# Kernel tuning notes

Hardware: AMD Instinct MI355X
Metric: run time of the kernel (lower is better)

The kernel has to match this reference:

```python
import jax, jax.numpy as jnp
import numpy as np

B, T, C = 64, 256, 64
E, H, HB, OUT = 32, 64, 128, 2


def setup_inputs() -> dict:
    key = jax.random.key(0)
    ks = iter(jax.random.split(key, 32))
    s = 0.02
    p = {}
    p["x"] = jax.random.normal(next(ks), (B, T, C), jnp.float32)
    # embedding Linear(1, E)
    p["embed_w"] = jax.random.normal(next(ks), (E, 1), jnp.float32) * s
    p["embed_b"] = jnp.zeros((E,), jnp.float32)
    # GRU (input E, hidden H); gate order r,z,n
    p["w_ih"] = jax.random.normal(next(ks), (3 * H, E), jnp.float32) * s
    p["w_hh"] = jax.random.normal(next(ks), (3 * H, H), jnp.float32) * s
    p["b_ih"] = jnp.zeros((3 * H,), jnp.float32)
    p["b_hh"] = jnp.zeros((3 * H,), jnp.float32)
    # BTP query / key MLPs: H->HB->HB->HB
    for nm in ("q", "k"):
        p[f"{nm}1_w"] = jax.random.normal(next(ks), (HB, H), jnp.float32) * s
        p[f"{nm}1_b"] = jnp.zeros((HB,), jnp.float32)
        p[f"{nm}2_w"] = jax.random.normal(next(ks), (HB, HB), jnp.float32) * s
        p[f"{nm}2_b"] = jnp.zeros((HB,), jnp.float32)
        p[f"{nm}3_w"] = jax.random.normal(next(ks), (HB, HB), jnp.float32) * s
        p[f"{nm}3_b"] = jnp.zeros((HB,), jnp.float32)
    # Gate bias (n_components x n_components), torch.randn init
    p["gate_bias"] = jax.random.normal(next(ks), (C, C), jnp.float32)
    # classifier: C^2 -> C^2/2 -> C^2/4 -> OUT
    d0, d1, d2 = C * C, C * C // 2, C * C // 4
    p["clf1_w"] = jax.random.normal(next(ks), (d1, d0), jnp.float32) * s
    p["clf1_b"] = jnp.zeros((d1,), jnp.float32)
    p["clf2_w"] = jax.random.normal(next(ks), (d2, d1), jnp.float32) * s
    p["clf2_b"] = jnp.zeros((d2,), jnp.float32)
    p["clf3_w"] = jax.random.normal(next(ks), (OUT, d2), jnp.float32) * s
    p["clf3_b"] = jnp.zeros((OUT,), jnp.float32)
    # predictor Linear(H, 1)
    p["pred_w"] = jax.random.normal(next(ks), (1, H), jnp.float32) * s
    p["pred_b"] = jnp.zeros((1,), jnp.float32)
    return p


def _mlp3(h, w1, b1, w2, b2, w3, b3):
    h = jax.nn.relu(h @ w1.T + b1)
    h = jax.nn.relu(h @ w2.T + b2)
    return h @ w3.T + b3


def reference(x, embed_w, embed_b, w_ih, w_hh, b_ih, b_hh,
              q1_w, q1_b, q2_w, q2_b, q3_w, q3_b,
              k1_w, k1_b, k2_w, k2_b, k3_w, k3_b,
              gate_bias, clf1_w, clf1_b, clf2_w, clf2_b, clf3_w, clf3_b,
              pred_w, pred_b):
    Bb, Tt, Cc = x.shape
    Hh = w_hh.shape[1]
    # embeddings: Linear(1,E) applied to each scalar -> [B,C,T,E]
    embedded = x.transpose(0, 2, 1)[..., None] * embed_w[:, 0] + embed_b
    xs = jnp.moveaxis(embedded, 2, 0)  # [T,B,C,E]

    def gru_cell(h, xt):
        gi = xt @ w_ih.T + b_ih           # [B,C,3H]
        gh = h @ w_hh.T + b_hh
        gi_r, gi_z, gi_n = jnp.split(gi, 3, axis=-1)
        gh_r, gh_z, gh_n = jnp.split(gh, 3, axis=-1)
        r = jax.nn.sigmoid(gi_r + gh_r)
        z = jax.nn.sigmoid(gi_z + gh_z)
        n = jnp.tanh(gi_n + r * gh_n)
        return (1.0 - z) * n + z * h

    def btp(h):
        q = _mlp3(h, q1_w, q1_b, q2_w, q2_b, q3_w, q3_b)   # [B,C,HB]
        k = _mlp3(h, k1_w, k1_b, k2_w, k2_b, k3_w, k3_b)
        transfer = jnp.einsum('bqd,bkd->bqk', q, k)        # [B,C,C]
        norms = jnp.sqrt(jnp.sum(transfer * transfer, axis=(1, 2), keepdims=True))
        transfer = transfer / norms
        gate = jax.nn.sigmoid(jnp.abs(transfer) + gate_bias)
        transfer = transfer * gate
        next_states = jnp.einsum('bij,bjd->bid', transfer, h)
        return next_states, transfer

    def step(h, xt):
        h = gru_cell(h, xt)
        h, transfer = btp(h)
        return h, (h, transfer)

    h0 = jnp.zeros((Bb, Cc, Hh), x.dtype)
    _, (hs, mats) = jax.lax.scan(step, h0, xs)
    hidden_states = jnp.moveaxis(hs, 0, 1)    # [B,T,C,H]
    matrices = jnp.moveaxis(mats, 0, 1)       # [B,T,C,C]

    # predictor on hidden states at t=0..T-2 -> predicts x[:,1:,:]
    predicted = (hidden_states[:, :-1] @ pred_w.T + pred_b)[..., 0]  # [B,T-1,C]

    clf_in = matrices.reshape(Bb, Tt, Cc * Cc)
    h1 = jax.nn.relu(clf_in @ clf1_w.T + clf1_b)   # dropout is identity in eval
    h2 = jax.nn.relu(h1 @ clf2_w.T + clf2_b)
    time_logits = h2 @ clf3_w.T + clf3_b            # [B,T,OUT]
    logits = jnp.mean(time_logits, axis=1)          # [B,OUT]
    return logits, matrices, time_logits, predicted, x[:, 1:, :]
```

## Files before the change

kernel.cpp:

```cpp
#include <hip/hip_runtime.h>
#include <hip/hip_bf16.h>
#include <math.h>

#define B_BATCH 64
#define T_STEPS 256
#define C_COMP  64

#define WSW_BYTE_OFF 2048
#define WHH_OFF 0
#define Q1_OFF 12288
#define K1_OFF 20480
#define Q2_OFF 28672
#define K2_OFF 45056
#define Q3_OFF 61440
#define K3_OFF 77824
#define C1WB_BYTE 262144
#define C2WB_BYTE 17039360
#define H1B_BYTE  21233664
#define H2B_BYTE  88342528
#define MB16_BYTE 121896960ULL

#define MAT_OFF  128
#define TL_OFF   67108992
#define PRED_OFF 67141760
#define XC_OFF   68186240

#define GST 196
#define HS  68
#define TS  68
#define GBS 68

typedef __attribute__((ext_vector_type(8))) short short8;
typedef __attribute__((ext_vector_type(4))) float f32x4;
#define MFMA16(a,b,c) __builtin_amdgcn_mfma_f32_16x16x32_bf16(a,b,c,0,0,0)

__device__ __forceinline__ float fsigm(float v) {
    return __builtin_amdgcn_rcpf(1.0f + __expf(-v));
}
__device__ __forceinline__ float ftanh(float v) {
    return 1.0f - 2.0f * __builtin_amdgcn_rcpf(__expf(2.0f * v) + 1.0f);
}
__device__ __forceinline__ short f2bs(float f) {
    unsigned u = __float_as_uint(f);
    u += 0x7fffu + ((u >> 16) & 1u);
    return (short)(u >> 16);
}
__device__ __forceinline__ float bf2f(short s) {
    return __uint_as_float(((unsigned)(unsigned short)s) << 16);
}
__device__ __forceinline__ unsigned pk2(float a, float b) {
    return (unsigned)(unsigned short)f2bs(a) | ((unsigned)(unsigned short)f2bs(b) << 16);
}
__device__ __forceinline__ void bar_lds() {
    asm volatile("s_waitcnt lgkmcnt(0)" ::: "memory");
    __builtin_amdgcn_s_barrier();
}
__device__ __forceinline__ int xorr(int row) { return ((row >> 1) & 7) << 3; }

__device__ __forceinline__ void async16(void* lds, const void* g) {
    __builtin_amdgcn_global_load_lds((const __attribute__((address_space(1))) void*)g,
                                     (__attribute__((address_space(3))) void*)lds, 16, 0, 0);
}

__global__ void precompute_kernel(const float* __restrict__ w_ih,
                                  const float* __restrict__ embed_w,
                                  const float* __restrict__ embed_b,
                                  const float* __restrict__ b_ih,
                                  float* __restrict__ avec, float* __restrict__ cvec)
{
    int g = threadIdx.x;
    if (g < 192) {
        float a = 0.f, c = 0.f;
        for (int e = 0; e < 32; ++e) {
            float w = w_ih[g * 32 + e];
            a += w * embed_w[e];
            c += w * embed_b[e];
        }
        avec[g] = a;
        cvec[g] = c + b_ih[g];
    }
}

__global__ void tobf16_kernel(const float* __restrict__ src, short* __restrict__ dst, int n)
{
    int i = blockIdx.x * 256 + threadIdx.x;
    if (i < n) dst[i] = f2bs(src[i]);
}

__global__ void expand_kernel(const short* __restrict__ mb, float* __restrict__ mat)
{
    const size_t i = ((size_t)blockIdx.x * 256 + threadIdx.x) * 8;
    short8 v = *(const short8*)&mb[i];
    float4 lo, hi;
    lo.x = bf2f(v[0]); lo.y = bf2f(v[1]); lo.z = bf2f(v[2]); lo.w = bf2f(v[3]);
    hi.x = bf2f(v[4]); hi.y = bf2f(v[5]); hi.z = bf2f(v[6]); hi.w = bf2f(v[7]);
    *reinterpret_cast<float4*>(&mat[i])     = lo;
    *reinterpret_cast<float4*>(&mat[i + 4]) = hi;
}

template<int KST, int AST, bool RELU>
__device__ __forceinline__ void two_strip_sw(
    const short* __restrict__ A,
    const short8* __restrict__ B0, const short8* __restrict__ B1,
    const f32x4 bias0, const f32x4 bias1,
    short* __restrict__ outb, const int s0, const int s1, const int ln, const int lh)
{
    f32x4 acc0[4], acc1[4];
#pragma unroll
    for (int g = 0; g < 4; ++g) { acc0[g] = bias0; acc1[g] = bias1; }
#pragma unroll
    for (int kk = 0; kk < KST; ++kk)
#pragma unroll
        for (int g = 0; g < 4; ++g) {
            const int row = g * 16 + ln;
            short8 a = *(const short8*)&A[row * AST + ((kk * 32 + lh * 8) ^ xorr(row))];
            acc0[g] = MFMA16(B0[kk], a, acc0[g]);
            acc1[g] = MFMA16(B1[kk], a, acc1[g]);
        }
#pragma unroll
    for (int g = 0; g < 4; ++g) {
        const int row = g * 16 + ln;
        f32x4 v0 = acc0[g], v1 = acc1[g];
        if (RELU) {
#pragma unroll
            for (int q = 0; q < 4; ++q) { v0[q] = fmaxf(v0[q], 0.f); v1[q] = fmaxf(v1[q], 0.f); }
        }
        uint2 p0, p1;
        p0.x = pk2(v0[0], v0[1]); p0.y = pk2(v0[2], v0[3]);
        p1.x = pk2(v1[0], v1[1]); p1.y = pk2(v1[2], v1[3]);
        *(uint2*)&outb[row * 128 + ((s0 * 16 + lh * 4) ^ xorr(row))] = p0;
        *(uint2*)&outb[row * 128 + ((s1 * 16 + lh * 4) ^ xorr(row))] = p1;
    }
}

__global__ __launch_bounds__(512) void scan_kernel(
    const float* __restrict__ x, const float* __restrict__ b_hh,
    const float* __restrict__ avec, const float* __restrict__ cvec,
    const short* __restrict__ wsw,
    const float* __restrict__ q1b, const float* __restrict__ q2b, const float* __restrict__ q3b,
    const float* __restrict__ k1b, const float* __restrict__ k2b, const float* __restrict__ k3b,
    const float* __restrict__ gate_bias,
    const float* __restrict__ pred_w, const float* __restrict__ pred_b,
    float* __restrict__ matrices, float* __restrict__ predicted,
    short* __restrict__ mb16, const int use_mb16)
{
    __shared__ __align__(16) short hb  [64 * 64];
    __shared__ __align__(16) short hbN [64 * 64];
    __shared__ __align__(16) short hbT [64 * 64];
    __shared__ __align__(16) float h32 [64 * HS];
    __shared__ __align__(16) short qf  [64 * 128];
    __shared__ __align__(16) short kf  [64 * 128];
    __shared__ __align__(16) float gbias_s[64 * GBS];
    __shared__ __align__(16) char arena[65536];
    __shared__ __align__(16) float avec_s[192];
    __shared__ __align__(16) float cvec_s[192];
    __shared__ __align__(16) float bhh_s[192];
    __shared__ __align__(16) float pw_s[64];
    __shared__ __align__(16) float xrow[64];
    __shared__ __align__(16) float red[8];

    float* gates = (float*)arena;
    short* act2q = (short*)arena;
    short* act2k = (short*)(arena + 16384);
    short* act1q = (short*)(arena + 32768);
    short* act1k = (short*)(arena + 49152);
    float* tf    = (float*)arena;
    short* tb    = (short*)(arena + 20480);

    const int tid = threadIdx.x;
    const int b = blockIdx.x;
    const int w = tid >> 6, lane = tid & 63;
    const int ln = lane & 15, lh = lane >> 4;
    const int path = w >> 2;
    const int wq = w & 3;

    for (int i = tid; i < 64 * 64; i += 512) { hb[i] = 0; hbN[i] = 0; hbT[i] = 0; }
    for (int i = tid; i < 64 * HS; i += 512) h32[i] = 0.f;
    for (int i = tid; i < 4096; i += 512)
        gbias_s[(i >> 6) * GBS + (i & 63)] = gate_bias[i];
    if (tid < 192) { avec_s[tid] = avec[tid]; cvec_s[tid] = cvec[tid]; bhh_s[tid] = b_hh[tid]; }
    if (tid < 64) { pw_s[tid] = pred_w[tid]; xrow[tid] = x[(size_t)b * T_STEPS * 64 + tid]; }
    const float pbv = pred_b[0];

    const short* whh_b = wsw + WHH_OFF;
    const short* l1w = path ? wsw + K1_OFF : wsw + Q1_OFF;
    const short* l2w = path ? wsw + K2_OFF : wsw + Q2_OFF;
    const short* l3w = path ? wsw + K3_OFF : wsw + Q3_OFF;
    const float* l1b = path ? k1b : q1b;
    const float* l2b = path ? k2b : q2b;
    const float* l3b = path ? k3b : q3b;

    short8 Bg[2][2], B1[2][2], B2[2][4], B3[2][4];
#pragma unroll
    for (int kk = 0; kk < 2; ++kk)
        Bg[0][kk] = *(const short8*)&whh_b[(w * 16 + ln) * 64 + kk * 32 + lh * 8];
    if (w < 4) {
#pragma unroll
        for (int kk = 0; kk < 2; ++kk)
            Bg[1][kk] = *(const short8*)&whh_b[((w + 8) * 16 + ln) * 64 + kk * 32 + lh * 8];
    }
#pragma unroll
    for (int s = 0; s < 2; ++s) {
        const int strip = wq + s * 4;
#pragma unroll
        for (int kk = 0; kk < 2; ++kk)
            B1[s][kk] = *(const short8*)&l1w[(strip * 16 + ln) * 64 + kk * 32 + lh * 8];
#pragma unroll
        for (int kk = 0; kk < 4; ++kk) {
            B2[s][kk] = *(const short8*)&l2w[(strip * 16 + ln) * 128 + kk * 32 + lh * 8];
            B3[s][kk] = *(const short8*)&l3w[(strip * 16 + ln) * 128 + kk * 32 + lh * 8];
        }
    }
    const f32x4 b1v0 = *(const f32x4*)&l1b[wq * 16 + lh * 4];
    const f32x4 b1v1 = *(const f32x4*)&l1b[(wq + 4) * 16 + lh * 4];
    const f32x4 b2v0 = *(const f32x4*)&l2b[wq * 16 + lh * 4];
    const f32x4 b2v1 = *(const f32x4*)&l2b[(wq + 4) * 16 + lh * 4];
    const f32x4 b3v0 = *(const f32x4*)&l3b[wq * 16 + lh * 4];
    const f32x4 b3v1 = *(const f32x4*)&l3b[(wq + 4) * 16 + lh * 4];
    __syncthreads();

    for (int t = 0; t < T_STEPS; ++t) {
        float xnext = 0.f;
        if (tid < 64 && t + 1 < T_STEPS)
            xnext = x[((size_t)b * T_STEPS + t + 1) * 64 + tid];
        if (t > 0) {
            const int c = tid >> 3, j0 = (tid & 7) * 8;
            f32x4 h0 = *(const f32x4*)&h32[c * HS + j0];
            f32x4 h1 = *(const f32x4*)&h32[c * HS + j0 + 4];
            f32x4 w0 = *(const f32x4*)&pw_s[j0];
            f32x4 w1 = *(const f32x4*)&pw_s[j0 + 4];
            float p = 0.f;
#pragma unroll
            for (int q = 0; q < 4; ++q) p = fmaf(h0[q], w0[q], fmaf(h1[q], w1[q], p));
            p += __shfl_xor(p, 1); p += __shfl_xor(p, 2); p += __shfl_xor(p, 4);
            if ((lane & 7) == 0)
                predicted[((size_t)b * (T_STEPS - 1) + (t - 1)) * 64 + c] = p + pbv;
        }
        {
            f32x4 accA[4], accB[4];
            const f32x4 bhA = *(const f32x4*)&bhh_s[w * 16 + lh * 4];
#pragma unroll
            for (int g = 0; g < 4; ++g) accA[g] = bhA;
            if (w < 4) {
                const f32x4 bhB = *(const f32x4*)&bhh_s[(w + 8) * 16 + lh * 4];
#pragma unroll
                for (int g = 0; g < 4; ++g) accB[g] = bhB;
            }
#pragma unroll
            for (int kk = 0; kk < 2; ++kk)
#pragma unroll
                for (int g = 0; g < 4; ++g) {
                    const int row = g * 16 + ln;
                    short8 hv = *(const short8*)&hb[row * 64 + ((kk * 32 + lh * 8) ^ xorr(row))];
                    accA[g] = MFMA16(Bg[0][kk], hv, accA[g]);
                    if (w < 4) accB[g] = MFMA16(Bg[1][kk], hv, accB[g]);
                }
#pragma unroll
            for (int g = 0; g < 4; ++g)
                *(f32x4*)&gates[(g * 16 + ln) * GST + w * 16 + lh * 4] = accA[g];
            if (w < 4) {
#pragma unroll
                for (int g = 0; g < 4; ++g)
                    *(f32x4*)&gates[(g * 16 + ln) * GST + (w + 8) * 16 + lh * 4] = accB[g];
            }
        }
        bar_lds();

        {
            const int c = tid >> 3, j0 = (tid & 7) * 8;
            const float xv = xrow[c];
            unsigned pk[4];
#pragma unroll
            for (int h2 = 0; h2 < 2; ++h2) {
                const int jh = j0 + h2 * 4;
                f32x4 gr4 = *(const f32x4*)&gates[c * GST + jh];
                f32x4 gz4 = *(const f32x4*)&gates[c * GST + 64 + jh];
                f32x4 gn4 = *(const f32x4*)&gates[c * GST + 128 + jh];
                f32x4 ho4 = *(const f32x4*)&h32[c * HS + jh];
                f32x4 ar4 = *(const f32x4*)&avec_s[jh];
                f32x4 az4 = *(const f32x4*)&avec_s[64 + jh];
                f32x4 an4 = *(const f32x4*)&avec_s[128 + jh];
                f32x4 cr4 = *(const f32x4*)&cvec_s[jh];
                f32x4 cz4 = *(const f32x4*)&cvec_s[64 + jh];
                f32x4 cn4 = *(const f32x4*)&cvec_s[128 + jh];
                f32x4 hn4;
#pragma unroll
                for (int q = 0; q < 4; ++q) {
                    const float r = fsigm(gr4[q] + fmaf(xv, ar4[q], cr4[q]));
                    const float z = fsigm(gz4[q] + fmaf(xv, az4[q], cz4[q]));
                    const float n = ftanh(fmaf(r, gn4[q], fmaf(xv, an4[q], cn4[q])));
                    hn4[q] = fmaf(z, ho4[q] - n, n);
                }
                *(f32x4*)&h32[c * HS + jh] = hn4;
                const unsigned plo = pk2(hn4[0], hn4[1]);
                const unsigned phi = pk2(hn4[2], hn4[3]);
                pk[h2 * 2] = plo; pk[h2 * 2 + 1] = phi;
                hbT[(jh + 0) * 64 + (c ^ xorr(jh + 0))] = (short)plo;
                hbT[(jh + 1) * 64 + (c ^ xorr(jh + 1))] = (short)(plo >> 16);
                hbT[(jh + 2) * 64 + (c ^ xorr(jh + 2))] = (short)phi;
                hbT[(jh + 3) * 64 + (c ^ xorr(jh + 3))] = (short)(phi >> 16);
            }
            uint4 pv; pv.x = pk[0]; pv.y = pk[1]; pv.z = pk[2]; pv.w = pk[3];
            *(uint4*)&hbN[c * 64 + (j0 ^ xorr(c))] = pv;
        }
        bar_lds();

        two_strip_sw<2, 64,  true >(hbN, B1[0], B1[1], b1v0, b1v1,
                                    path ? act1k : act1q, wq, wq + 4, ln, lh);
        bar_lds();
        two_strip_sw<4, 128, true >(path ? act1k : act1q, B2[0], B2[1], b2v0, b2v1,
                                    path ? act2k : act2q, wq, wq + 4, ln, lh);
        bar_lds();
        two_strip_sw<4, 128, false>(path ? act2k : act2q, B3[0], B3[1], b3v0, b3v1,
                                    path ? kf : qf, wq, wq + 4, ln, lh);
        bar_lds();

        {
            const int qg = w & 3, kg = (w >> 2) * 2;
            f32x4 ac0 = {0,0,0,0}, ac1 = {0,0,0,0};
#pragma unroll
            for (int kk = 0; kk < 4; ++kk) {
                const int rq = qg * 16 + ln, rk0 = kg * 16 + ln, rk1 = (kg + 1) * 16 + ln;
                short8 bq = *(const short8*)&qf[rq * 128 + ((kk * 32 + lh * 8) ^ xorr(rq))];
                short8 a0 = *(const short8*)&kf[rk0 * 128 + ((kk * 32 + lh * 8) ^ xorr(rk0))];
                short8 a1 = *(const short8*)&kf[rk1 * 128 + ((kk * 32 + lh * 8) ^ xorr(rk1))];
                ac0 = MFMA16(a0, bq, ac0);
                ac1 = MFMA16(a1, bq, ac1);
            }
            const int qrow = qg * 16 + ln;
            *(f32x4*)&tf[qrow * TS + kg * 16 + lh * 4]       = ac0;
            *(f32x4*)&tf[qrow * TS + (kg + 1) * 16 + lh * 4] = ac1;
            float ss = 0.f;
#pragma unroll
            for (int q = 0; q < 4; ++q)
                ss = fmaf(ac0[q], ac0[q], fmaf(ac1[q], ac1[q], ss));
#pragma unroll
            for (int off = 1; off < 64; off <<= 1) ss += __shfl_xor(ss, off);
            if (lane == 0) red[w] = ss;
            if (tid < 64 && t + 1 < T_STEPS) xrow[tid] = xnext;
        }
        bar_lds();

        {
            const int ci = tid >> 3, j0 = (tid & 7) * 8;
            const float ssum = red[0]+red[1]+red[2]+red[3]+red[4]+red[5]+red[6]+red[7];
            const float inv = __builtin_amdgcn_rsqf(ssum);
            const size_t mbase = ((size_t)b * T_STEPS + t) * 4096;
            unsigned pk[4];
#pragma unroll
            for (int h2 = 0; h2 < 2; ++h2) {
                const int jh = j0 + h2 * 4;
                f32x4 t4  = *(const f32x4*)&tf[ci * TS + jh];
                f32x4 gb4 = *(const f32x4*)&gbias_s[ci * GBS + jh];
                f32x4 v4;
#pragma unroll
                for (int q = 0; q < 4; ++q) {
                    const float tv = t4[q] * inv;
                    const float g = fsigm(fabsf(tv) + gb4[q]);
                    v4[q] = tv * g;
                }
                pk[h2 * 2]     = pk2(v4[0], v4[1]);
                pk[h2 * 2 + 1] = pk2(v4[2], v4[3]);
                if (!use_mb16)
                    *(f32x4*)&matrices[mbase + ci * 64 + jh] = v4;
            }
            uint4 pv; pv.x = pk[0]; pv.y = pk[1]; pv.z = pk[2]; pv.w = pk[3];
            if (use_mb16)
                *(uint4*)&mb16[mbase + ci * 64 + j0] = pv;
            *(uint4*)&tb[ci * 64 + (j0 ^ xorr(ci))] = pv;
        }
        bar_lds();

        {
            const int jg = w & 3, ig = (w >> 2) * 2;
            f32x4 hc0 = {0,0,0,0}, hc1 = {0,0,0,0};
#pragma unroll
            for (int kk = 0; kk < 2; ++kk) {
                const int rj = jg * 16 + ln, ri0 = ig * 16 + ln, ri1 = (ig + 1) * 16 + ln;
                short8 bt = *(const short8*)&tb [rj * 64 + ((kk * 32 + lh * 8) ^ xorr(rj))];
                short8 a0 = *(const short8*)&hbT[ri0 * 64 + ((kk * 32 + lh * 8) ^ xorr(ri0))];
                short8 a1 = *(const short8*)&hbT[ri1 * 64 + ((kk * 32 + lh * 8) ^ xorr(ri1))];
                hc0 = MFMA16(a0, bt, hc0);
                hc1 = MFMA16(a1, bt, hc1);
            }
            const int row = jg * 16 + ln;
            *(f32x4*)&h32[row * HS + ig * 16 + lh * 4]       = hc0;
            *(f32x4*)&h32[row * HS + (ig + 1) * 16 + lh * 4] = hc1;
            uint2 p0, p1;
            p0.x = pk2(hc0[0], hc0[1]); p0.y = pk2(hc0[2], hc0[3]);
            p1.x = pk2(hc1[0], hc1[1]); p1.y = pk2(hc1[2], hc1[3]);
            *(uint2*)&hb[row * 64 + ((ig * 16 + lh * 4) ^ xorr(row))]       = p0;
            *(uint2*)&hb[row * 64 + (((ig + 1) * 16 + lh * 4) ^ xorr(row))] = p1;
        }
        bar_lds();
    }
}

__global__ void copyx_kernel(const float* __restrict__ x, float* __restrict__ out5)
{
    int i = blockIdx.x * 256 + threadIdx.x;
    if (i < B_BATCH * (T_STEPS - 1) * C_COMP) {
        int b = i / ((T_STEPS - 1) * C_COMP);
        int r = i - b * (T_STEPS - 1) * C_COMP;
        out5[i] = x[(size_t)b * (T_STEPS * C_COMP) + r + C_COMP];
    }
}

__global__ __launch_bounds__(256) void gemm1_kernel(
    const float* __restrict__ A, const short* __restrict__ Bw,
    const float* __restrict__ bias, short* __restrict__ Cb,
    const int M, const int N, const int K)
{
    __shared__ __align__(16) short Asb[128 * 64];
    __shared__ __align__(16) short Bsb[128 * 64];
    const int tid = threadIdx.x;
    const int w = tid >> 6, lane = tid & 63;
    const int ln = lane & 15, lh = lane >> 4;
    const int wr = w >> 1, wc = w & 1;

    const int ntc = N >> 7;
    const int g = blockIdx.x;
    const int xcd = g & 7, chunk = g >> 3;
    const int mt = xcd * ((M >> 7) >> 3) + chunk / ntc;
    const int nt = chunk % ntc;
    const int m0 = mt << 7, n0 = nt << 7;

    const int ar = tid >> 1;
    const int ac = (tid & 1) << 5;
    const short* bsrc = Bw + (size_t)(n0 + w * 32 + (lane >> 3)) * K + ((lane & 7) << 3);
    short* bdst = &Bsb[w * 32 * 64 + lane * 8];

    f32x4 acc[4][4];
#pragma unroll
    for (int m = 0; m < 4; ++m)
#pragma unroll
        for (int n = 0; n < 4; ++n) acc[m][n] = (f32x4){0, 0, 0, 0};

    for (int k0 = 0; k0 < K; k0 += 64) {
        const float* arow = A + (size_t)(m0 + ar) * K + k0 + ac;
        float4 av[8];
#pragma unroll
        for (int i = 0; i < 8; ++i) av[i] = *reinterpret_cast<const float4*>(arow + i * 4);
        short8 cv[4];
#pragma unroll
        for (int i = 0; i < 4; ++i) {
            cv[i][0] = f2bs(av[2*i].x);   cv[i][1] = f2bs(av[2*i].y);
            cv[i][2] = f2bs(av[2*i].z);   cv[i][3] = f2bs(av[2*i].w);
            cv[i][4] = f2bs(av[2*i+1].x); cv[i][5] = f2bs(av[2*i+1].y);
            cv[i][6] = f2bs(av[2*i+1].z); cv[i][7] = f2bs(av[2*i+1].w);
        }
        __syncthreads();
#pragma unroll
        for (int i = 0; i < 4; ++i)
            *reinterpret_cast<short8*>(&Asb[ar * 64 + ac + i * 8]) = cv[i];
#pragma unroll
        for (int i = 0; i < 4; ++i)
            async16(bdst + i * 512, bsrc + (size_t)i * 8 * K + k0);
        __syncthreads();
#pragma unroll
        for (int kk = 0; kk < 2; ++kk) {
            short8 af[4], bfr[4];
#pragma unroll
            for (int m = 0; m < 4; ++m)
                af[m] = *reinterpret_cast<const short8*>(&Asb[(wr*64 + m*16 + ln)*64 + kk*32 + lh*8]);
#pragma unroll
            for (int n = 0; n < 4; ++n)
                bfr[n] = *reinterpret_cast<const short8*>(&Bsb[(wc*64 + n*16 + ln)*64 + kk*32 + lh*8]);
#pragma unroll
            for (int m = 0; m < 4; ++m)
#pragma unroll
                for (int n = 0; n < 4; ++n)
                    acc[m][n] = MFMA16(af[m], bfr[n], acc[m][n]);
        }
    }
#pragma unroll
    for (int n = 0; n < 4; ++n) {
        const int col = n0 + wc * 64 + n * 16 + ln;
        const float bv = bias[col];
#pragma unroll
        for (int m = 0; m < 4; ++m)
#pragma unroll
            for (int q = 0; q < 4; ++q) {
                const int row = m0 + wr * 64 + m * 16 + lh * 4 + q;
                Cb[(size_t)row * N + col] = f2bs(fmaxf(acc[m][n][q] + bv, 0.f));
            }
    }
}

__global__ __launch_bounds__(256) void gemm2_kernel(
    const short* __restrict__ Ab, const short* __restrict__ Bw,
    const float* __restrict__ bias, short* __restrict__ Cb,
    const int M, const int N, const int K)
{
    __shared__ __align__(16) short Asb[128 * 64];
    __shared__ __align__(16) short Bsb[128 * 64];
    const int tid = threadIdx.x;
    const int w = tid >> 6, lane = tid & 63;
    const int ln = lane & 15, lh = lane >> 4;
    const int wr = w >> 1, wc = w & 1;

    const int ntc = N >> 7;
    const int g = blockIdx.x;
    const int xcd = g & 7, chunk = g >> 3;
    const int mt = xcd * ((M >> 7) >> 3) + chunk / ntc;
    const int nt = chunk % ntc;
    const int m0 = mt << 7, n0 = nt << 7;

    const short* asrc = Ab + (size_t)(m0 + w * 32 + (lane >> 3)) * K + ((lane & 7) << 3);
    const short* bsrc = Bw + (size_t)(n0 + w * 32 + (lane >> 3)) * K + ((lane & 7) << 3);
    short* adst = &Asb[w * 32 * 64 + lane * 8];
    short* bdst = &Bsb[w * 32 * 64 + lane * 8];

    f32x4 acc[4][4];
#pragma unroll
    for (int m = 0; m < 4; ++m)
#pragma unroll
        for (int n = 0; n < 4; ++n) acc[m][n] = (f32x4){0, 0, 0, 0};

    for (int k0 = 0; k0 < K; k0 += 64) {
        __syncthreads();
#pragma unroll
        for (int i = 0; i < 4; ++i) {
            async16(adst + i * 512, asrc + (size_t)i * 8 * K + k0);
            async16(bdst + i * 512, bsrc + (size_t)i * 8 * K + k0);
        }
        __syncthreads();
#pragma unroll
        for (int kk = 0; kk < 2; ++kk) {
            short8 af[4], bfr[4];
#pragma unroll
            for (int m = 0; m < 4; ++m)
                af[m] = *reinterpret_cast<const short8*>(&Asb[(wr*64 + m*16 + ln)*64 + kk*32 + lh*8]);
#pragma unroll
            for (int n = 0; n < 4; ++n)
                bfr[n] = *reinterpret_cast<const short8*>(&Bsb[(wc*64 + n*16 + ln)*64 + kk*32 + lh*8]);
#pragma unroll
            for (int m = 0; m < 4; ++m)
#pragma unroll
                for (int n = 0; n < 4; ++n)
                    acc[m][n] = MFMA16(af[m], bfr[n], acc[m][n]);
        }
    }
#pragma unroll
    for (int n = 0; n < 4; ++n) {
        const int col = n0 + wc * 64 + n * 16 + ln;
        const float bv = bias[col];
#pragma unroll
        for (int m = 0; m < 4; ++m)
#pragma unroll
            for (int q = 0; q < 4; ++q) {
                const int row = m0 + wr * 64 + m * 16 + lh * 4 + q;
                Cb[(size_t)row * N + col] = f2bs(fmaxf(acc[m][n][q] + bv, 0.f));
            }
    }
}

__global__ __launch_bounds__(256) void clf3_kernel(const short* __restrict__ h2b,
    const float* __restrict__ w3, const float* __restrict__ b3, float* __restrict__ TL)
{
    const int lane = threadIdx.x & 63;
    const int w = threadIdx.x >> 6;
    const size_t r = (size_t)blockIdx.x * 4 + w;
    const short* hr = h2b + r * 1024;
    float a0 = 0.f, a1 = 0.f;
#pragma unroll
    for (int half = 0; half < 2; ++half) {
        const int k = half * 512 + lane * 8;
        short8 hv = *(const short8*)&hr[k];
#pragma unroll
        for (int u = 0; u < 8; ++u) {
            const float hf = bf2f(hv[u]);
            a0 = fmaf(hf, w3[k + u], a0);
            a1 = fmaf(hf, w3[1024 + k + u], a1);
        }
    }
    for (int off = 32; off; off >>= 1) { a0 += __shfl_xor(a0, off); a1 += __shfl_xor(a1, off); }
    if (lane == 0) {
        TL[r * 2 + 0] = a0 + b3[0];
        TL[r * 2 + 1] = a1 + b3[1];
    }
}

__global__ void logits_kernel(const float* __restrict__ TL, float* __restrict__ out)
{
    const int tid = threadIdx.x;
    if (tid >= 128) return;
    const int b = tid >> 1, o = tid & 1;
    float s = 0.f;
    for (int t = 0; t < T_STEPS; ++t) s += TL[((size_t)b * T_STEPS + t) * 2 + o];
    out[b * 2 + o] = s * (1.0f / 256.0f);
}

extern "C" void kernel_launch(void* const* d_in, const int* in_sizes, int n_in,
                              void* d_out, int out_size, void* d_ws, size_t ws_size,
                              hipStream_t stream)
{
    const float* x       = (const float*)d_in[0];
    const float* embed_w = (const float*)d_in[1];
    const float* embed_b = (const float*)d_in[2];
    const float* w_ih    = (const float*)d_in[3];
    const float* w_hh    = (const float*)d_in[4];
    const float* b_ih    = (const float*)d_in[5];
    const float* b_hh    = (const float*)d_in[6];
    const float* q1w = (const float*)d_in[7],  *q1b = (const float*)d_in[8];
    const float* q2w = (const float*)d_in[9],  *q2b = (const float*)d_in[10];
    const float* q3w = (const float*)d_in[11], *q3b = (const float*)d_in[12];
    const float* k1w = (const float*)d_in[13], *k1b = (const float*)d_in[14];
    const float* k2w = (const float*)d_in[15], *k2b = (const float*)d_in[16];
    const float* k3w = (const float*)d_in[17], *k3b = (const float*)d_in[18];
    const float* gate_bias = (const float*)d_in[19];
    const float* c1w = (const float*)d_in[20], *c1b = (const float*)d_in[21];
    const float* c2w = (const float*)d_in[22], *c2b = (const float*)d_in[23];
    const float* c3w = (const float*)d_in[24], *c3b = (const float*)d_in[25];
    const float* pw  = (const float*)d_in[26], *pb  = (const float*)d_in[27];

    float* out       = (float*)d_out;
    float* logits    = out;
    float* matrices  = out + MAT_OFF;
    float* TL        = out + TL_OFF;
    float* predicted = out + PRED_OFF;
    float* xcopy     = out + XC_OFF;

    float* ws   = (float*)d_ws;
    float* avec = ws;
    float* cvec = ws + 192;
    short* wsw  = (short*)((char*)d_ws + WSW_BYTE_OFF);
    short* c1wb = (short*)((char*)d_ws + C1WB_BYTE);
    short* c2wb = (short*)((char*)d_ws + C2WB_BYTE);
    short* h1b  = (short*)((char*)d_ws + H1B_BYTE);
    short* h2b  = (short*)((char*)d_ws + H2B_BYTE);

    const int use_mb16 = (ws_size >= MB16_BYTE + 134217728ULL) ? 1 : 0;
    short* mb16 = use_mb16 ? (short*)((char*)d_ws + MB16_BYTE) : (short*)d_ws;

    precompute_kernel<<<1, 256, 0, stream>>>(w_ih, embed_w, embed_b, b_ih, avec, cvec);

    tobf16_kernel<<<(12288 + 255) / 256, 256, 0, stream>>>(w_hh, wsw + WHH_OFF, 12288);
    tobf16_kernel<<<(8192  + 255) / 256, 256, 0, stream>>>(q1w,  wsw + Q1_OFF,  8192);
    tobf16_kernel<<<(8192  + 255) / 256, 256, 0, stream>>>(k1w,  wsw + K1_OFF,  8192);
    tobf16_kernel<<<(16384 + 255) / 256, 256, 0, stream>>>(q2w,  wsw + Q2_OFF,  16384);
    tobf16_kernel<<<(16384 + 255) / 256, 256, 0, stream>>>(k2w,  wsw + K2_OFF,  16384);
    tobf16_kernel<<<(16384 + 255) / 256, 256, 0, stream>>>(q3w,  wsw + Q3_OFF,  16384);
    tobf16_kernel<<<(16384 + 255) / 256, 256, 0, stream>>>(k3w,  wsw + K3_OFF,  16384);
    tobf16_kernel<<<(2048 * 4096 + 255) / 256, 256, 0, stream>>>(c1w, c1wb, 2048 * 4096);
    tobf16_kernel<<<(1024 * 2048 + 255) / 256, 256, 0, stream>>>(c2w, c2wb, 1024 * 2048);

    scan_kernel<<<B_BATCH, 512, 0, stream>>>(x, b_hh, avec, cvec, wsw,
        q1b, q2b, q3b, k1b, k2b, k3b, gate_bias, pw, pb, matrices, predicted,
        mb16, use_mb16);

    if (use_mb16)
        expand_kernel<<<32768, 256, 0, stream>>>(mb16, matrices);

    copyx_kernel<<<(B_BATCH * (T_STEPS - 1) * C_COMP + 255) / 256, 256, 0, stream>>>(x, xcopy);

    const int Mtot = B_BATCH * T_STEPS;
    if (use_mb16) {
        gemm2_kernel<<<(Mtot / 128) * (2048 / 128), 256, 0, stream>>>(
            mb16, c1wb, c1b, h1b, Mtot, 2048, 4096);
    } else {
        gemm1_kernel<<<(Mtot / 128) * (2048 / 128), 256, 0, stream>>>(
            matrices, c1wb, c1b, h1b, Mtot, 2048, 4096);
    }
    gemm2_kernel<<<(Mtot / 128) * (1024 / 128), 256, 0, stream>>>(
        h1b, c2wb, c2b, h2b, Mtot, 1024, 2048);
    clf3_kernel<<<Mtot / 4, 256, 0, stream>>>(h2b, c3w, c3b, TL);
    logits_kernel<<<1, 128, 0, stream>>>(TL, logits);
}
```

Measured before the change: 2.770 ms.

## Merge bf16 weight conversions into one vectorized kernel and drop expand pass

Result: faster. 2.688 ms (-3.0%).

```diff
diff --git a/kernel.cpp b/kernel.cpp
--- a/kernel.cpp
+++ b/kernel.cpp
@@ -81,21 +81,33 @@
     }
 }
 
-__global__ void tobf16_kernel(const float* __restrict__ src, short* __restrict__ dst, int n)
-{
-    int i = blockIdx.x * 256 + threadIdx.x;
-    if (i < n) dst[i] = f2bs(src[i]);
-}
-
-__global__ void expand_kernel(const short* __restrict__ mb, float* __restrict__ mat)
-{
-    const size_t i = ((size_t)blockIdx.x * 256 + threadIdx.x) * 8;
-    short8 v = *(const short8*)&mb[i];
-    float4 lo, hi;
-    lo.x = bf2f(v[0]); lo.y = bf2f(v[1]); lo.z = bf2f(v[2]); lo.w = bf2f(v[3]);
-    hi.x = bf2f(v[4]); hi.y = bf2f(v[5]); hi.z = bf2f(v[6]); hi.w = bf2f(v[7]);
-    *reinterpret_cast<float4*>(&mat[i])     = lo;
-    *reinterpret_cast<float4*>(&mat[i + 4]) = hi;
+__global__ __launch_bounds__(256) void tobf16_all_kernel(
+    const float* __restrict__ s_whh,
+    const float* __restrict__ s_q1, const float* __restrict__ s_k1,
+    const float* __restrict__ s_q2, const float* __restrict__ s_k2,
+    const float* __restrict__ s_q3, const float* __restrict__ s_k3,
+    const float* __restrict__ s_c1, const float* __restrict__ s_c2,
+    short* __restrict__ wsw, short* __restrict__ c1wb, short* __restrict__ c2wb)
+{
+    int bb = blockIdx.x;
+    const float* src; short* dst; int n;
+    if      (bb < 12)   { src = s_whh; dst = wsw + WHH_OFF; n = 12288;            }
+    else if (bb < 20)   { src = s_q1;  dst = wsw + Q1_OFF;  n = 8192;  bb -= 12;  }
+    else if (bb < 28)   { src = s_k1;  dst = wsw + K1_OFF;  n = 8192;  bb -= 20;  }
+    else if (bb < 44)   { src = s_q2;  dst = wsw + Q2_OFF;  n = 16384; bb -= 28;  }
+    else if (bb < 60)   { src = s_k2;  dst = wsw + K2_OFF;  n = 16384; bb -= 44;  }
+    else if (bb < 76)   { src = s_q3;  dst = wsw + Q3_OFF;  n = 16384; bb -= 60;  }
+    else if (bb < 92)   { src = s_k3;  dst = wsw + K3_OFF;  n = 16384; bb -= 76;  }
+    else if (bb < 8284) { src = s_c1;  dst = c1wb;          n = 8388608; bb -= 92; }
+    else                { src = s_c2;  dst = c2wb;          n = 2097152; bb -= 8284; }
+    const int i = bb * 1024 + threadIdx.x * 4;
+    if (i < n) {
+        float4 v = *reinterpret_cast<const float4*>(&src[i]);
+        uint2 p;
+        p.x = pk2(v.x, v.y);
+        p.y = pk2(v.z, v.w);
+        *reinterpret_cast<uint2*>(&dst[i]) = p;
+    }
 }
 
 template<int KST, int AST, bool RELU>
@@ -361,8 +373,7 @@
                 }
                 pk[h2 * 2]     = pk2(v4[0], v4[1]);
                 pk[h2 * 2 + 1] = pk2(v4[2], v4[3]);
-                if (!use_mb16)
-                    *(f32x4*)&matrices[mbase + ci * 64 + jh] = v4;
+                *(f32x4*)&matrices[mbase + ci * 64 + jh] = v4;
             }
             uint4 pv; pv.x = pk[0]; pv.y = pk[1]; pv.z = pk[2]; pv.w = pk[3];
             if (use_mb16)
@@ -635,22 +646,12 @@
 
     precompute_kernel<<<1, 256, 0, stream>>>(w_ih, embed_w, embed_b, b_ih, avec, cvec);
 
-    tobf16_kernel<<<(12288 + 255) / 256, 256, 0, stream>>>(w_hh, wsw + WHH_OFF, 12288);
-    tobf16_kernel<<<(8192  + 255) / 256, 256, 0, stream>>>(q1w,  wsw + Q1_OFF,  8192);
-    tobf16_kernel<<<(8192  + 255) / 256, 256, 0, stream>>>(k1w,  wsw + K1_OFF,  8192);
-    tobf16_kernel<<<(16384 + 255) / 256, 256, 0, stream>>>(q2w,  wsw + Q2_OFF,  16384);
-    tobf16_kernel<<<(16384 + 255) / 256, 256, 0, stream>>>(k2w,  wsw + K2_OFF,  16384);
-    tobf16_kernel<<<(16384 + 255) / 256, 256, 0, stream>>>(q3w,  wsw + Q3_OFF,  16384);
-    tobf16_kernel<<<(16384 + 255) / 256, 256, 0, stream>>>(k3w,  wsw + K3_OFF,  16384);
-    tobf16_kernel<<<(2048 * 4096 + 255) / 256, 256, 0, stream>>>(c1w, c1wb, 2048 * 4096);
-    tobf16_kernel<<<(1024 * 2048 + 255) / 256, 256, 0, stream>>>(c2w, c2wb, 1024 * 2048);
+    tobf16_all_kernel<<<10332, 256, 0, stream>>>(
+        w_hh, q1w, k1w, q2w, k2w, q3w, k3w, c1w, c2w, wsw, c1wb, c2wb);
 
     scan_kernel<<<B_BATCH, 512, 0, stream>>>(x, b_hh, avec, cvec, wsw,
         q1b, q2b, q3b, k1b, k2b, k3b, gate_bias, pw, pb, matrices, predicted,
         mb16, use_mb16);
-
-    if (use_mb16)
-        expand_kernel<<<32768, 256, 0, stream>>>(mb16, matrices);
 
     copyx_kernel<<<(B_BATCH * (T_STEPS - 1) * C_COMP + 255) / 256, 256, 0, stream>>>(x, xcopy);
 
```
